# Kernel tuning notes

Measured on AMD Instinct MI355X. Metric: run time of the kernel, lower is better.

## Reference

```python
import jax, jax.numpy as jnp
import numpy as np

N = 512          # input_size (reservoir dim)
B = 16384        # batch
OUT = 256        # output_size
MAX_ITER = 64    # reservoir_config['max_iter']
LEAK = 0.9       # reservoir_config['leak_rate']
RHO = 0.9        # reservoir_config['spectral_radius']
TOL = 1e-6       # early-stop threshold on norm(x)/x.shape[0]


def setup_inputs() -> dict:
    key = jax.random.key(0)
    k1, k2, k3 = jax.random.split(key, 3)
    x = jax.random.normal(k1, (B, N), dtype=jnp.float32)
    # reservoir = randn(N,N) scaled so its spectral radius == RHO (as in __init__)
    W = np.asarray(jax.random.normal(k2, (N, N), dtype=jnp.float32))
    ev = np.linalg.eigvals(W)
    W = W / np.abs(ev).max() * RHO
    # readout: nn.Linear(N, OUT, bias=False) weight, shape (OUT, N)
    w_out = jax.random.normal(k3, (OUT, N), dtype=jnp.float32) / np.sqrt(N).astype(np.float32)
    return {"x": x, "reservoir": jnp.asarray(W, dtype=jnp.float32), "w_out": w_out}


def reference(x, reservoir, w_out):
    # one leaky update is always applied before the loop in the torch code
    def step(h):
        return LEAK * h + (1.0 - LEAK) * (h @ reservoir)

    x = step(x)

    # loop of up to MAX_ITER further updates; early-stop when norm(x)/B < TOL.
    # scan with a masked (where) update is the jit-friendly, differentiable
    # equivalent of the Python break: once the condition trips, x is frozen.
    def body(h, _):
        keep_going = jnp.linalg.norm(h) / h.shape[0] >= TOL
        h = jnp.where(keep_going, step(h), h)
        return h, None

    x, _ = jax.lax.scan(body, x, None, length=MAX_ITER)

    # readout: bias-free linear
    return x @ w_out.T
```

## Files before the change

### kernel.cpp

```cpp
#include <hip/hip_runtime.h>


typedef __attribute__((ext_vector_type(4))) float f32x4;
typedef __attribute__((ext_vector_type(8))) short bf16x8;
typedef __attribute__((ext_vector_type(4))) unsigned short u16x4;

typedef __attribute__((address_space(1))) const unsigned int guint;
typedef __attribute__((address_space(3))) unsigned int luint;

__device__ __forceinline__ void gld_lds16(const void* g, void* l) {
    __builtin_amdgcn_global_load_lds((guint*)g, (luint*)l, 16, 0, 0);
}

__device__ __forceinline__ unsigned short f2bf(float f) {
    unsigned int u = __float_as_uint(f);
    return (unsigned short)((u + 0x7fffu + ((u >> 16) & 1u)) >> 16);
}
__device__ __forceinline__ float bf2f(unsigned short h) {
    return __uint_as_float(((unsigned int)h) << 16);
}
__device__ __forceinline__ void split2(float v, unsigned short& h, unsigned short& l) {
    h = f2bf(v);
    l = f2bf(v - bf2f(h));
}

__global__ __launch_bounds__(256) void build_M(const float* __restrict__ W,
        unsigned short* __restrict__ Mh, unsigned short* __restrict__ Ml,
        unsigned short* __restrict__ MTh, unsigned short* __restrict__ MTl) {
    __shared__ unsigned short Lh[32][40], Ll[32][40];
    const int tid = threadIdx.x, bid = blockIdx.x;
    const int row0 = (bid >> 4) << 5, col0 = (bid & 15) << 5;
    const int r = tid >> 3, c4 = (tid & 7) << 2;
    f32x4 v = *(const f32x4*)&W[(row0 + r) * 512 + col0 + c4];
    u16x4 h4, l4;
    #pragma unroll
    for (int j = 0; j < 4; ++j) {
        float val = 0.1f * v[j];
        if (row0 + r == col0 + c4 + j) val += 0.9f;
        unsigned short hh, ll; split2(val, hh, ll);
        h4[j] = hh; l4[j] = ll;
    }
    *(u16x4*)&Mh[(row0 + r) * 512 + col0 + c4] = h4;
    *(u16x4*)&Ml[(row0 + r) * 512 + col0 + c4] = l4;
    *(u16x4*)&Lh[r][c4] = h4;
    *(u16x4*)&Ll[r][c4] = l4;
    __syncthreads();
    const int c = tid >> 3, rr = (tid & 7) << 2;
    u16x4 th, tl;
    #pragma unroll
    for (int j = 0; j < 4; ++j) { th[j] = Lh[rr + j][c]; tl[j] = Ll[rr + j][c]; }
    *(u16x4*)&MTh[(col0 + c) * 512 + row0 + rr] = th;
    *(u16x4*)&MTl[(col0 + c) * 512 + row0 + rr] = tl;
}

__global__ __launch_bounds__(256) void wsplit(const float* __restrict__ w,
        unsigned short* __restrict__ WOh, unsigned short* __restrict__ WOl) {
    const int i4 = (blockIdx.x * 256 + threadIdx.x) * 4;
    f32x4 v = *(const f32x4*)&w[i4];
    u16x4 h4, l4;
    #pragma unroll
    for (int j = 0; j < 4; ++j) { unsigned short hh, ll; split2(v[j], hh, ll); h4[j] = hh; l4[j] = ll; }
    *(u16x4*)&WOh[i4] = h4;
    *(u16x4*)&WOl[i4] = l4;
}

template<int NC, int OUTMODE>
__global__ __launch_bounds__(256) void chain_mm2(
        const unsigned short* __restrict__ Agh, const unsigned short* __restrict__ Agl,
        const unsigned short* __restrict__ BTh, const unsigned short* __restrict__ BTl,
        unsigned short* __restrict__ Ch, unsigned short* __restrict__ Cl,
        unsigned short* __restrict__ CTh, unsigned short* __restrict__ CTl) {
    __shared__ unsigned short SB[2][4][32][64];
    const int tid = threadIdx.x, lane = tid & 63, w = tid >> 6;
    const int wr = w >> 1, wc = w & 1;
    const int l16 = lane & 15, ks = lane >> 4;
    const int row0 = (NC == 512 ? (blockIdx.x >> 4) : (blockIdx.x >> 3)) << 5;
    const int col0 = (NC == 512 ? (blockIdx.x & 15) : (blockIdx.x & 7)) << 5;

    const int srow = tid >> 3;
    const int ssw  = ((tid & 7) << 4) ^ ((srow & 7) << 4);
    const unsigned short* aghp = Agh + (row0 + srow) * 512 + (ssw >> 1);
    const unsigned short* aglp = Agl + (row0 + srow) * 512 + (ssw >> 1);
    const unsigned short* bthp = BTh + (col0 + srow) * 512 + (ssw >> 1);
    const unsigned short* btlp = BTl + (col0 + srow) * 512 + (ssw >> 1);

    f32x4 acc0 = {}, acc1 = {};

    #define CH_STAGE(buf, t) {                                        \
        const int k_ = (t) << 6;                                      \
        char* d_ = (char*)SB[buf][0] + tid * 16;                      \
        gld_lds16(aghp + k_, d_);                                     \
        gld_lds16(aglp + k_, d_ + 4096);                              \
        gld_lds16(bthp + k_, d_ + 8192);                              \
        gld_lds16(btlp + k_, d_ + 12288);                             \
    }

    CH_STAGE(0, 0);
    #pragma unroll
    for (int t = 0; t < 8; ++t) {
        const int buf = t & 1;
        if (t < 7) CH_STAGE(buf ^ 1, t + 1);
        if (t < 7) asm volatile("s_waitcnt vmcnt(4)" ::: "memory");
        else       asm volatile("s_waitcnt vmcnt(0)" ::: "memory");
        __builtin_amdgcn_sched_barrier(0);
        __builtin_amdgcn_s_barrier();

        const int sw = (l16 & 7) << 4;
        const int ra = (wr * 16 + l16) * 128;
        const int rb = (wc * 16 + l16) * 128;
        #pragma unroll
        for (int s = 0; s < 2; ++s) {
            const int qa = (ra + s * 64 + ks * 16) ^ sw;
            const int qb = (rb + s * 64 + ks * 16) ^ sw;
            bf16x8 ah = *(const bf16x8*)((const char*)SB[buf][0] + qa);
            bf16x8 al = *(const bf16x8*)((const char*)SB[buf][1] + qa);
            bf16x8 bh = *(const bf16x8*)((const char*)SB[buf][2] + qb);
            bf16x8 bl = *(const bf16x8*)((const char*)SB[buf][3] + qb);
            acc0 = __builtin_amdgcn_mfma_f32_16x16x32_bf16(ah, bh, acc0, 0, 0, 0);
            acc1 = __builtin_amdgcn_mfma_f32_16x16x32_bf16(ah, bl, acc1, 0, 0, 0);
            acc1 = __builtin_amdgcn_mfma_f32_16x16x32_bf16(al, bh, acc1, 0, 0, 0);
        }
        __builtin_amdgcn_s_barrier();
    }
    #undef CH_STAGE

    const int orow = row0 + wr * 16 + ks * 4;
    const int ocol = col0 + wc * 16 + l16;
    float cv[4];
    #pragma unroll
    for (int j = 0; j < 4; ++j) cv[j] = acc0[j] + acc1[j];
    if (OUTMODE == 2) {
        u16x4 t4;
        #pragma unroll
        for (int j = 0; j < 4; ++j) t4[j] = f2bf(cv[j]);
        *(u16x4*)&CTh[ocol * 512 + orow] = t4;
    } else {
        u16x4 th4, tl4;
        #pragma unroll
        for (int j = 0; j < 4; ++j) {
            unsigned short hh, ll; split2(cv[j], hh, ll);
            th4[j] = hh; tl4[j] = ll;
            if (OUTMODE == 0) {
                Ch[(orow + j) * 512 + ocol] = hh;
                Cl[(orow + j) * 512 + ocol] = ll;
            }
        }
        *(u16x4*)&CTh[ocol * 512 + orow] = th4;
        *(u16x4*)&CTl[ocol * 512 + orow] = tl4;
    }
}

__global__ __launch_bounds__(256, 2) void gemm_final(const float* __restrict__ X,
        const unsigned short* __restrict__ Pt, float* __restrict__ out) {
    __shared__ float XS[2][32][64];
    const int tid = threadIdx.x, lane = tid & 63, w = tid >> 6;
    const int l16 = lane & 15, ks = lane >> 4;
    const int row0 = blockIdx.x << 5;

    const int srow = tid >> 4;
    const int scs  = (((tid & 15) << 4) ^ ((srow & 7) << 4)) >> 2;
    const float* xp0 = X + (row0 + srow) * 512 + scs;
    const float* xp1 = X + (row0 + 16 + srow) * 512 + scs;
    const unsigned short* bp = Pt + (w * 64 + l16) * 512 + ks * 8;

    f32x4 acc[2][4] = {};
    bf16x8 Breg[2][8];

    #define FG_STAGE(buf, t) {                                       \
        const int k_ = (t) << 6;                                     \
        gld_lds16(xp0 + k_, (char*)XS[buf] + tid * 16);              \
        gld_lds16(xp1 + k_, (char*)XS[buf] + 4096 + tid * 16);       \
    }
    #define FG_LOADB(set, t) {                                       \
        const int k_ = (t) << 6;                                     \
        _Pragma("unroll")                                            \
        for (int n = 0; n < 4; ++n)                                  \
            _Pragma("unroll")                                        \
            for (int s = 0; s < 2; ++s)                              \
                Breg[set][n * 2 + s] =                               \
                    *(const bf16x8*)&bp[n * 8192 + k_ + s * 32];     \
    }

    FG_STAGE(0, 0);
    FG_LOADB(0, 0);
    #pragma unroll
    for (int t = 0; t < 8; ++t) {
        const int buf = t & 1;
        if (t < 7) { FG_STAGE(buf ^ 1, t + 1); FG_LOADB(buf ^ 1, t + 1); }
        if (t < 7) asm volatile("s_waitcnt vmcnt(10)" ::: "memory");
        else       asm volatile("s_waitcnt vmcnt(0)" ::: "memory");
        __builtin_amdgcn_sched_barrier(0);
        __builtin_amdgcn_s_barrier();

        const int sw = (l16 & 7) << 4;
        #pragma unroll
        for (int m = 0; m < 2; ++m) {
            bf16x8 af[2];
            #pragma unroll
            for (int s = 0; s < 2; ++s) {
                const int q = (m * 16 + l16) * 256 + s * 128 + ks * 32;
                f32x4 v0 = *(const f32x4*)((const char*)XS[buf] + (q ^ sw));
                f32x4 v1 = *(const f32x4*)((const char*)XS[buf] + ((q + 16) ^ sw));
                #pragma unroll
                for (int j = 0; j < 4; ++j) {
                    af[s][j]     = (short)f2bf(v0[j]);
                    af[s][4 + j] = (short)f2bf(v1[j]);
                }
            }
            #pragma unroll
            for (int n = 0; n < 4; ++n) {
                acc[m][n] = __builtin_amdgcn_mfma_f32_16x16x32_bf16(af[0], Breg[buf][n * 2 + 0], acc[m][n], 0, 0, 0);
                acc[m][n] = __builtin_amdgcn_mfma_f32_16x16x32_bf16(af[1], Breg[buf][n * 2 + 1], acc[m][n], 0, 0, 0);
            }
        }
        __builtin_amdgcn_s_barrier();
    }
    #undef FG_STAGE
    #undef FG_LOADB

    #pragma unroll
    for (int m = 0; m < 2; ++m)
        #pragma unroll
        for (int n = 0; n < 4; ++n)
            #pragma unroll
            for (int j = 0; j < 4; ++j)
                out[(row0 + m * 16 + ks * 4 + j) * 256 + w * 64 + n * 16 + l16] = acc[m][n][j];
}

extern "C" void kernel_launch(void* const* d_in, const int* in_sizes, int n_in,
                              void* d_out, int out_size, void* d_ws, size_t ws_size,
                              hipStream_t stream) {
    const float* x     = (const float*)d_in[0];
    const float* W     = (const float*)d_in[1];
    const float* w_out = (const float*)d_in[2];
    float* out = (float*)d_out;
    unsigned short* u = (unsigned short*)d_ws;

    const size_t SZ = 512 * 512, HZ = 256 * 512;
    unsigned short *S0h = u,          *S0l = u + SZ,     *S0Th = u + 2 * SZ, *S0Tl = u + 3 * SZ;
    unsigned short *S1h = u + 4 * SZ, *S1l = u + 5 * SZ, *S1Th = u + 6 * SZ, *S1Tl = u + 7 * SZ;
    unsigned short *QTh = u + 8 * SZ, *QTl = QTh + HZ, *Ptb = QTl + HZ;
    unsigned short *WOh = Ptb + HZ,   *WOl = WOh + HZ;

    dim3 blk(256);
    wsplit <<<128, blk, 0, stream>>>(w_out, WOh, WOl);
    build_M<<<256, blk, 0, stream>>>(W, S0h, S0l, S0Th, S0Tl);
    chain_mm2<256, 1><<<128, blk, 0, stream>>>(S0h, S0l, WOh, WOl, nullptr, nullptr, QTh, QTl);
    chain_mm2<512, 0><<<256, blk, 0, stream>>>(S0h, S0l, S0Th, S0Tl, S1h, S1l, S1Th, S1Tl);
    chain_mm2<512, 0><<<256, blk, 0, stream>>>(S1h, S1l, S1Th, S1Tl, S0h, S0l, S0Th, S0Tl);
    chain_mm2<512, 0><<<256, blk, 0, stream>>>(S0h, S0l, S0Th, S0Tl, S1h, S1l, S1Th, S1Tl);
    chain_mm2<512, 0><<<256, blk, 0, stream>>>(S1h, S1l, S1Th, S1Tl, S0h, S0l, S0Th, S0Tl);
    chain_mm2<512, 0><<<256, blk, 0, stream>>>(S0h, S0l, S0Th, S0Tl, S1h, S1l, S1Th, S1Tl);
    chain_mm2<512, 0><<<256, blk, 0, stream>>>(S1h, S1l, S1Th, S1Tl, S0h, S0l, S0Th, S0Tl);
    chain_mm2<256, 2><<<128, blk, 0, stream>>>(S0h, S0l, QTh, QTl, nullptr, nullptr, Ptb, nullptr);
    gemm_final<<<512, blk, 0, stream>>>(x, Ptb, out);
}
```

Measured before the change: 137.7 us.

## Fuse reservoir power chain into one persistent kernel with grid barriers

Folds the split preprocessing, matrix-squaring chain and final products into a single 256-block persistent kernel. The blocks synchronise through atomic-counter grid barriers, which removes about ten kernel launches and their gaps. Each tile now loads the full K=512 slab into 128KB of LDS at once instead of double-buffering, and uses three separate accumulators. gemm_final is split into a 2D grid with half the columns per block so more blocks fit per CU. The grid barrier depends on all 256 blocks being co-resident, which is risky with 128KB of LDS per block, and adds a memset launch.

```diff
diff --git a/kernel.cpp b/kernel.cpp
--- a/kernel.cpp
+++ b/kernel.cpp
@@ -2,6 +2,7 @@
 
 
 typedef __attribute__((ext_vector_type(4))) float f32x4;
+typedef __attribute__((ext_vector_type(2))) float f32x2;
 typedef __attribute__((ext_vector_type(8))) short bf16x8;
 typedef __attribute__((ext_vector_type(4))) unsigned short u16x4;
 
@@ -24,111 +25,62 @@
     l = f2bf(v - bf2f(h));
 }
 
-__global__ __launch_bounds__(256) void build_M(const float* __restrict__ W,
-        unsigned short* __restrict__ Mh, unsigned short* __restrict__ Ml,
-        unsigned short* __restrict__ MTh, unsigned short* __restrict__ MTl) {
-    __shared__ unsigned short Lh[32][40], Ll[32][40];
-    const int tid = threadIdx.x, bid = blockIdx.x;
-    const int row0 = (bid >> 4) << 5, col0 = (bid & 15) << 5;
-    const int r = tid >> 3, c4 = (tid & 7) << 2;
-    f32x4 v = *(const f32x4*)&W[(row0 + r) * 512 + col0 + c4];
-    u16x4 h4, l4;
-    #pragma unroll
-    for (int j = 0; j < 4; ++j) {
-        float val = 0.1f * v[j];
-        if (row0 + r == col0 + c4 + j) val += 0.9f;
-        unsigned short hh, ll; split2(val, hh, ll);
-        h4[j] = hh; l4[j] = ll;
-    }
-    *(u16x4*)&Mh[(row0 + r) * 512 + col0 + c4] = h4;
-    *(u16x4*)&Ml[(row0 + r) * 512 + col0 + c4] = l4;
-    *(u16x4*)&Lh[r][c4] = h4;
-    *(u16x4*)&Ll[r][c4] = l4;
+__device__ __forceinline__ void gbar(int* cnt, int idx) {
     __syncthreads();
-    const int c = tid >> 3, rr = (tid & 7) << 2;
-    u16x4 th, tl;
-    #pragma unroll
-    for (int j = 0; j < 4; ++j) { th[j] = Lh[rr + j][c]; tl[j] = Ll[rr + j][c]; }
-    *(u16x4*)&MTh[(col0 + c) * 512 + row0 + rr] = th;
-    *(u16x4*)&MTl[(col0 + c) * 512 + row0 + rr] = tl;
-}
-
-__global__ __launch_bounds__(256) void wsplit(const float* __restrict__ w,
-        unsigned short* __restrict__ WOh, unsigned short* __restrict__ WOl) {
-    const int i4 = (blockIdx.x * 256 + threadIdx.x) * 4;
-    f32x4 v = *(const f32x4*)&w[i4];
-    u16x4 h4, l4;
-    #pragma unroll
-    for (int j = 0; j < 4; ++j) { unsigned short hh, ll; split2(v[j], hh, ll); h4[j] = hh; l4[j] = ll; }
-    *(u16x4*)&WOh[i4] = h4;
-    *(u16x4*)&WOl[i4] = l4;
-}
-
-template<int NC, int OUTMODE>
-__global__ __launch_bounds__(256) void chain_mm2(
+    if (threadIdx.x == 0) {
+        __threadfence();
+        atomicAdd(&cnt[idx], 1);
+        while (atomicAdd(&cnt[idx], 0) < 256) __builtin_amdgcn_s_sleep(2);
+        __threadfence();
+    }
+    __syncthreads();
+}
+
+template<int OUTMODE>
+__device__ __forceinline__ void mm_tile(
         const unsigned short* __restrict__ Agh, const unsigned short* __restrict__ Agl,
         const unsigned short* __restrict__ BTh, const unsigned short* __restrict__ BTl,
         unsigned short* __restrict__ Ch, unsigned short* __restrict__ Cl,
-        unsigned short* __restrict__ CTh, unsigned short* __restrict__ CTl) {
-    __shared__ unsigned short SB[2][4][32][64];
+        unsigned short* __restrict__ CTh, unsigned short* __restrict__ CTl,
+        int row0, int col0, char* lds) {
     const int tid = threadIdx.x, lane = tid & 63, w = tid >> 6;
-    const int wr = w >> 1, wc = w & 1;
-    const int l16 = lane & 15, ks = lane >> 4;
-    const int row0 = (NC == 512 ? (blockIdx.x >> 4) : (blockIdx.x >> 3)) << 5;
-    const int col0 = (NC == 512 ? (blockIdx.x & 15) : (blockIdx.x & 7)) << 5;
-
-    const int srow = tid >> 3;
-    const int ssw  = ((tid & 7) << 4) ^ ((srow & 7) << 4);
-    const unsigned short* aghp = Agh + (row0 + srow) * 512 + (ssw >> 1);
-    const unsigned short* aglp = Agl + (row0 + srow) * 512 + (ssw >> 1);
-    const unsigned short* bthp = BTh + (col0 + srow) * 512 + (ssw >> 1);
-    const unsigned short* btlp = BTl + (col0 + srow) * 512 + (ssw >> 1);
-
-    f32x4 acc0 = {}, acc1 = {};
-
-    #define CH_STAGE(buf, t) {                                        \
-        const int k_ = (t) << 6;                                      \
-        char* d_ = (char*)SB[buf][0] + tid * 16;                      \
-        gld_lds16(aghp + k_, d_);                                     \
-        gld_lds16(aglp + k_, d_ + 4096);                              \
-        gld_lds16(bthp + k_, d_ + 8192);                              \
-        gld_lds16(btlp + k_, d_ + 12288);                             \
-    }
-
-    CH_STAGE(0, 0);
-    #pragma unroll
-    for (int t = 0; t < 8; ++t) {
-        const int buf = t & 1;
-        if (t < 7) CH_STAGE(buf ^ 1, t + 1);
-        if (t < 7) asm volatile("s_waitcnt vmcnt(4)" ::: "memory");
-        else       asm volatile("s_waitcnt vmcnt(0)" ::: "memory");
-        __builtin_amdgcn_sched_barrier(0);
-        __builtin_amdgcn_s_barrier();
-
-        const int sw = (l16 & 7) << 4;
-        const int ra = (wr * 16 + l16) * 128;
-        const int rb = (wc * 16 + l16) * 128;
-        #pragma unroll
-        for (int s = 0; s < 2; ++s) {
-            const int qa = (ra + s * 64 + ks * 16) ^ sw;
-            const int qb = (rb + s * 64 + ks * 16) ^ sw;
-            bf16x8 ah = *(const bf16x8*)((const char*)SB[buf][0] + qa);
-            bf16x8 al = *(const bf16x8*)((const char*)SB[buf][1] + qa);
-            bf16x8 bh = *(const bf16x8*)((const char*)SB[buf][2] + qb);
-            bf16x8 bl = *(const bf16x8*)((const char*)SB[buf][3] + qb);
-            acc0 = __builtin_amdgcn_mfma_f32_16x16x32_bf16(ah, bh, acc0, 0, 0, 0);
-            acc1 = __builtin_amdgcn_mfma_f32_16x16x32_bf16(ah, bl, acc1, 0, 0, 0);
-            acc1 = __builtin_amdgcn_mfma_f32_16x16x32_bf16(al, bh, acc1, 0, 0, 0);
-        }
-        __builtin_amdgcn_s_barrier();
-    }
-    #undef CH_STAGE
-
-    const int orow = row0 + wr * 16 + ks * 4;
+    const int wr = w >> 1, wc = w & 1, l16 = lane & 15, ks = lane >> 4;
+    const int t6 = tid >> 6, c64 = (tid & 63) << 4;
+    #pragma unroll
+    for (int i = 0; i < 8; ++i) {
+        const int r = (i << 2) + t6;
+        const int gcol = (c64 ^ ((r & 7) << 4)) >> 1;
+        char* d = lds + (i << 12) + (tid << 4);
+        gld_lds16(Agh + (row0 + r) * 512 + gcol, d);
+        gld_lds16(Agl + (row0 + r) * 512 + gcol, d + 32768);
+        gld_lds16(BTh + (col0 + r) * 512 + gcol, d + 65536);
+        gld_lds16(BTl + (col0 + r) * 512 + gcol, d + 98304);
+    }
+    asm volatile("s_waitcnt vmcnt(0)" ::: "memory");
+    __builtin_amdgcn_sched_barrier(0);
+    __builtin_amdgcn_s_barrier();
+
+    f32x4 acc0 = {}, acc1 = {}, acc2 = {};
+    const int sw = (l16 & 7) << 4;
+    const int ra = (wr * 16 + l16) << 10;
+    const int rb = (wc * 16 + l16) << 10;
+    #pragma unroll
+    for (int s = 0; s < 16; ++s) {
+        const int qo = ((s << 6) + (ks << 4)) ^ sw;
+        bf16x8 ah = *(const bf16x8*)(lds + ra + qo);
+        bf16x8 al = *(const bf16x8*)(lds + 32768 + ra + qo);
+        bf16x8 bh = *(const bf16x8*)(lds + 65536 + rb + qo);
+        bf16x8 bl = *(const bf16x8*)(lds + 98304 + rb + qo);
+        acc0 = __builtin_amdgcn_mfma_f32_16x16x32_bf16(ah, bh, acc0, 0, 0, 0);
+        acc1 = __builtin_amdgcn_mfma_f32_16x16x32_bf16(ah, bl, acc1, 0, 0, 0);
+        acc2 = __builtin_amdgcn_mfma_f32_16x16x32_bf16(al, bh, acc2, 0, 0, 0);
+    }
+
+    const int orow = row0 + wr * 16 + (ks << 2);
     const int ocol = col0 + wc * 16 + l16;
     float cv[4];
     #pragma unroll
-    for (int j = 0; j < 4; ++j) cv[j] = acc0[j] + acc1[j];
+    for (int j = 0; j < 4; ++j) cv[j] = acc0[j] + acc1[j] + acc2[j];
     if (OUTMODE == 2) {
         u16x4 t4;
         #pragma unroll
@@ -150,21 +102,87 @@
     }
 }
 
-__global__ __launch_bounds__(256, 2) void gemm_final(const float* __restrict__ X,
+__global__ __launch_bounds__(256) void reservoir_chain(
+        const float* __restrict__ W, const float* __restrict__ wo,
+        unsigned short* __restrict__ u, int* __restrict__ cnt) {
+    __shared__ __align__(128) char lds[131072];
+    const int tid = threadIdx.x, bid = blockIdx.x;
+
+    const size_t SZ = 512 * 512;
+    unsigned short *SMh = u,           *SMl = u + SZ,     *SMTh = u + 2 * SZ, *SMTl = u + 3 * SZ;
+    unsigned short *S0h = u + 4 * SZ,  *S0l = u + 5 * SZ, *S0Th = u + 6 * SZ, *S0Tl = u + 7 * SZ;
+    unsigned short *S1h = u + 8 * SZ,  *S1l = u + 9 * SZ, *S1Th = u + 10 * SZ, *S1Tl = u + 11 * SZ;
+    unsigned short *WOh = u + 12 * SZ, *WOl = WOh + 131072;
+    unsigned short *QTh = u + 13 * SZ, *QTl = QTh + 131072;
+    unsigned short *Ptb = u + 14 * SZ;
+
+    {
+        unsigned short (*Lh)[40] = (unsigned short (*)[40])lds;
+        unsigned short (*Ll)[40] = (unsigned short (*)[40])(lds + 2560);
+        const int row0 = (bid >> 4) << 5, col0 = (bid & 15) << 5;
+        const int r = tid >> 3, c4 = (tid & 7) << 2;
+        f32x4 v = *(const f32x4*)&W[(row0 + r) * 512 + col0 + c4];
+        u16x4 h4, l4;
+        #pragma unroll
+        for (int j = 0; j < 4; ++j) {
+            float val = 0.1f * v[j];
+            if (row0 + r == col0 + c4 + j) val += 0.9f;
+            unsigned short hh, ll; split2(val, hh, ll);
+            h4[j] = hh; l4[j] = ll;
+        }
+        *(u16x4*)&SMh[(row0 + r) * 512 + col0 + c4] = h4;
+        *(u16x4*)&SMl[(row0 + r) * 512 + col0 + c4] = l4;
+        *(u16x4*)&Lh[r][c4] = h4;
+        *(u16x4*)&Ll[r][c4] = l4;
+        const int i2 = (bid << 9) + (tid << 1);
+        f32x2 wv = *(const f32x2*)&wo[i2];
+        unsigned short wh, wl;
+        split2(wv.x, wh, wl); WOh[i2] = wh;     WOl[i2] = wl;
+        split2(wv.y, wh, wl); WOh[i2 + 1] = wh; WOl[i2 + 1] = wl;
+        __syncthreads();
+        const int c = tid >> 3, rr = (tid & 7) << 2;
+        u16x4 th, tl;
+        #pragma unroll
+        for (int j = 0; j < 4; ++j) { th[j] = Lh[rr + j][c]; tl[j] = Ll[rr + j][c]; }
+        *(u16x4*)&SMTh[(col0 + c) * 512 + row0 + rr] = th;
+        *(u16x4*)&SMTl[(col0 + c) * 512 + row0 + rr] = tl;
+    }
+    gbar(cnt, 0);
+
+    const int sr0 = (bid >> 4) << 5, sc0 = (bid & 15) << 5;
+    mm_tile<0>(SMh, SMl, SMTh, SMTl, S0h, S0l, S0Th, S0Tl, sr0, sc0, lds); gbar(cnt, 1);
+    mm_tile<0>(S0h, S0l, S0Th, S0Tl, S1h, S1l, S1Th, S1Tl, sr0, sc0, lds); gbar(cnt, 2);
+    mm_tile<0>(S1h, S1l, S1Th, S1Tl, S0h, S0l, S0Th, S0Tl, sr0, sc0, lds); gbar(cnt, 3);
+    mm_tile<0>(S0h, S0l, S0Th, S0Tl, S1h, S1l, S1Th, S1Tl, sr0, sc0, lds); gbar(cnt, 4);
+    mm_tile<0>(S1h, S1l, S1Th, S1Tl, S0h, S0l, S0Th, S0Tl, sr0, sc0, lds); gbar(cnt, 5);
+    mm_tile<0>(S0h, S0l, S0Th, S0Tl, S1h, S1l, S1Th, S1Tl, sr0, sc0, lds); gbar(cnt, 6);
+
+    if (bid < 128) {
+        const int qr0 = (bid >> 3) << 5, qc0 = (bid & 7) << 5;
+        mm_tile<1>(SMh, SMl, WOh, WOl, nullptr, nullptr, QTh, QTl, qr0, qc0, lds);
+    }
+    gbar(cnt, 7);
+    if (bid < 128) {
+        const int qr0 = (bid >> 3) << 5, qc0 = (bid & 7) << 5;
+        mm_tile<2>(S1h, S1l, QTh, QTl, nullptr, nullptr, Ptb, nullptr, qr0, qc0, lds);
+    }
+}
+
+__global__ __launch_bounds__(256, 4) void gemm_final(const float* __restrict__ X,
         const unsigned short* __restrict__ Pt, float* __restrict__ out) {
     __shared__ float XS[2][32][64];
     const int tid = threadIdx.x, lane = tid & 63, w = tid >> 6;
     const int l16 = lane & 15, ks = lane >> 4;
-    const int row0 = blockIdx.x << 5;
+    const int row0 = blockIdx.y << 5, col0 = blockIdx.x << 7;
 
     const int srow = tid >> 4;
     const int scs  = (((tid & 15) << 4) ^ ((srow & 7) << 4)) >> 2;
     const float* xp0 = X + (row0 + srow) * 512 + scs;
     const float* xp1 = X + (row0 + 16 + srow) * 512 + scs;
-    const unsigned short* bp = Pt + (w * 64 + l16) * 512 + ks * 8;
-
-    f32x4 acc[2][4] = {};
-    bf16x8 Breg[2][8];
+    const unsigned short* bp = Pt + (col0 + w * 32 + l16) * 512 + ks * 8;
+
+    f32x4 acc[2][2] = {};
+    bf16x8 Breg[2][4];
 
     #define FG_STAGE(buf, t) {                                       \
         const int k_ = (t) << 6;                                     \
@@ -174,7 +192,7 @@
     #define FG_LOADB(set, t) {                                       \
         const int k_ = (t) << 6;                                     \
         _Pragma("unroll")                                            \
-        for (int n = 0; n < 4; ++n)                                  \
+        for (int n = 0; n < 2; ++n)                                  \
             _Pragma("unroll")                                        \
             for (int s = 0; s < 2; ++s)                              \
                 Breg[set][n * 2 + s] =                               \
@@ -187,7 +205,7 @@
     for (int t = 0; t < 8; ++t) {
         const int buf = t & 1;
         if (t < 7) { FG_STAGE(buf ^ 1, t + 1); FG_LOADB(buf ^ 1, t + 1); }
-        if (t < 7) asm volatile("s_waitcnt vmcnt(10)" ::: "memory");
+        if (t < 7) asm volatile("s_waitcnt vmcnt(6)" ::: "memory");
         else       asm volatile("s_waitcnt vmcnt(0)" ::: "memory");
         __builtin_amdgcn_sched_barrier(0);
         __builtin_amdgcn_s_barrier();
@@ -208,7 +226,7 @@
                 }
             }
             #pragma unroll
-            for (int n = 0; n < 4; ++n) {
+            for (int n = 0; n < 2; ++n) {
                 acc[m][n] = __builtin_amdgcn_mfma_f32_16x16x32_bf16(af[0], Breg[buf][n * 2 + 0], acc[m][n], 0, 0, 0);
                 acc[m][n] = __builtin_amdgcn_mfma_f32_16x16x32_bf16(af[1], Breg[buf][n * 2 + 1], acc[m][n], 0, 0, 0);
             }
@@ -221,10 +239,10 @@
     #pragma unroll
     for (int m = 0; m < 2; ++m)
         #pragma unroll
-        for (int n = 0; n < 4; ++n)
+        for (int n = 0; n < 2; ++n)
             #pragma unroll
             for (int j = 0; j < 4; ++j)
-                out[(row0 + m * 16 + ks * 4 + j) * 256 + w * 64 + n * 16 + l16] = acc[m][n][j];
+                out[(row0 + m * 16 + ks * 4 + j) * 256 + col0 + w * 32 + n * 16 + l16] = acc[m][n][j];
 }
 
 extern "C" void kernel_launch(void* const* d_in, const int* in_sizes, int n_in,
@@ -236,22 +254,11 @@
     float* out = (float*)d_out;
     unsigned short* u = (unsigned short*)d_ws;
 
-    const size_t SZ = 512 * 512, HZ = 256 * 512;
-    unsigned short *S0h = u,          *S0l = u + SZ,     *S0Th = u + 2 * SZ, *S0Tl = u + 3 * SZ;
-    unsigned short *S1h = u + 4 * SZ, *S1l = u + 5 * SZ, *S1Th = u + 6 * SZ, *S1Tl = u + 7 * SZ;
-    unsigned short *QTh = u + 8 * SZ, *QTl = QTh + HZ, *Ptb = QTl + HZ;
-    unsigned short *WOh = Ptb + HZ,   *WOl = WOh + HZ;
-
-    dim3 blk(256);
-    wsplit <<<128, blk, 0, stream>>>(w_out, WOh, WOl);
-    build_M<<<256, blk, 0, stream>>>(W, S0h, S0l, S0Th, S0Tl);
-    chain_mm2<256, 1><<<128, blk, 0, stream>>>(S0h, S0l, WOh, WOl, nullptr, nullptr, QTh, QTl);
-    chain_mm2<512, 0><<<256, blk, 0, stream>>>(S0h, S0l, S0Th, S0Tl, S1h, S1l, S1Th, S1Tl);
-    chain_mm2<512, 0><<<256, blk, 0, stream>>>(S1h, S1l, S1Th, S1Tl, S0h, S0l, S0Th, S0Tl);
-    chain_mm2<512, 0><<<256, blk, 0, stream>>>(S0h, S0l, S0Th, S0Tl, S1h, S1l, S1Th, S1Tl);
-    chain_mm2<512, 0><<<256, blk, 0, stream>>>(S1h, S1l, S1Th, S1Tl, S0h, S0l, S0Th, S0Tl);
-    chain_mm2<512, 0><<<256, blk, 0, stream>>>(S0h, S0l, S0Th, S0Tl, S1h, S1l, S1Th, S1Tl);
-    chain_mm2<512, 0><<<256, blk, 0, stream>>>(S1h, S1l, S1Th, S1Tl, S0h, S0l, S0Th, S0Tl);
-    chain_mm2<256, 2><<<128, blk, 0, stream>>>(S0h, S0l, QTh, QTl, nullptr, nullptr, Ptb, nullptr);
-    gemm_final<<<512, blk, 0, stream>>>(x, Ptb, out);
-}
+    const size_t SZ = 512 * 512;
+    unsigned short* Ptb = u + 14 * SZ;
+    int* cnt = (int*)(u + 15 * SZ);
+
+    hipMemsetAsync(cnt, 0, 128, stream);
+    reservoir_chain<<<256, 256, 0, stream>>>(W, w_out, u, cnt);
+    gemm_final<<<dim3(2, 512), 256, 0, stream>>>(x, Ptb, out);
+}
```

Measured after the change: 298.0 us. 2.16x slower.
